# Optimization experiments

Hardware: AMD Instinct MI355X
Metric: run time of the kernel (lower is better)

## Reference

```python
import jax, jax.numpy as jnp
import numpy as np

MAX_ITER = 10
EPSILON = 1e-4


def setup_inputs() -> dict:
    key = jax.random.key(0)
    k1, k2 = jax.random.split(key)
    B, N1, N2 = 128, 512, 512
    s = jax.random.uniform(k1, (B, N1, N2), dtype=jnp.float32)
    # per-sample effective sizes; original module assumes nrows[b] == ncols[b]
    nrows = jax.random.randint(k2, (B,), 256, N1 + 1, dtype=jnp.int32)
    ncols = nrows
    return {"s": s, "nrows": nrows, "ncols": ncols}


def reference(s, nrows, ncols):
    """Faithful BiStochastic (masked Sinkhorn) forward.

    Even iter i: column-normalize within the [ncols, ncols] top-left block,
    zero everything outside the block (matches s * tmp with tmp zero outside).
    Odd  iter i: row-normalize within the [nrows, nrows] block, zero outside.
    """
    B, n1, n2 = s.shape
    i1 = jnp.arange(n1)
    i2 = jnp.arange(n2)
    # masks derived from the block-ones matrices in the original code
    cmask_r = i1[None, :] < ncols[:, None]           # [B, n1] rows < ncols
    cmask_c = i2[None, :] < ncols[:, None]           # [B, n2] cols < ncols
    rmask_r = i1[None, :] < nrows[:, None]           # [B, n1] rows < nrows
    rmask_c = i2[None, :] < nrows[:, None]           # [B, n2] cols < nrows
    col_block = cmask_r[:, :, None] & cmask_c[:, None, :]  # [B, n1, n2]
    row_block = rmask_r[:, :, None] & rmask_c[:, None, :]  # [B, n1, n2]

    s = s + EPSILON
    for i in range(MAX_ITER):
        if i % 2 == 0:
            # col_sum[b, c] = sum_{r < ncols[b]} s[b, r, c]
            col_sum = jnp.sum(jnp.where(cmask_r[:, :, None], s, 0.0),
                              axis=1, keepdims=True)          # [B, 1, n2]
            denom = jnp.where(col_block, col_sum, 1.0)
            s = jnp.where(col_block, s, 0.0) / denom
        else:
            # row_sum[b, r] = sum_{c < nrows[b]} s[b, r, c]
            row_sum = jnp.sum(jnp.where(rmask_c[:, None, :], s, 0.0),
                              axis=2, keepdims=True)          # [B, n1, 1]
            denom = jnp.where(row_block, row_sum, 1.0)
            s = jnp.where(row_block, s, 0.0) / denom
    return s
```

## Files before the change

### kernel.cpp

```cpp
#include <hip/hip_runtime.h>

#define N     512
#define NSP   4
#define SC    128
#define MROW  65
#define EPS   1e-4f

#define LDS_U   (512 * MROW + 512 + 128 * 33 + 128 + 64)
#define LDS_BYTES (LDS_U * 4)

union U32H { unsigned int u; _Float16 h[2]; };
__device__ inline float h_lo(unsigned int x){ U32H t; t.u = x; return (float)t.h[0]; }
__device__ inline float h_hi(unsigned int x){ U32H t; t.u = x; return (float)t.h[1]; }
__device__ inline unsigned int h_pk(float a, float b){ U32H t; t.h[0]=(_Float16)a; t.h[1]=(_Float16)b; return t.u; }

typedef _Float16 half2v __attribute__((ext_vector_type(2)));
#if __has_builtin(__builtin_amdgcn_fdot2)
__device__ inline float dot2(unsigned int m, unsigned int v, float c){
    return __builtin_amdgcn_fdot2(__builtin_bit_cast(half2v, m), __builtin_bit_cast(half2v, v), c, false);
}
#else
__device__ inline float dot2(unsigned int m, unsigned int v, float c){
    return c + h_lo(m)*h_lo(v) + h_hi(m)*h_hi(v);
}
#endif

__device__ inline void pass_tail(unsigned int* M2, float* red, float* vf, unsigned int* vpk,
                                 const float acc[8], int t, int part, int j, int c0, int n,
                                 int b, int sp, float* __restrict__ rp_out,
                                 float* __restrict__ vf_out) {
#pragma unroll
    for (int k = 0; k < 8; ++k) red[(8*j + k)*33 + part] = acc[k];
    __syncthreads();
    if (t < 128) {
        float s = 0.f;
#pragma unroll
        for (int p = 0; p < 32; ++p) s += red[t*33 + p];
        float v = (c0 + t < n) ? 1.f / s : 0.f;
        vf[t] = v;
        if (vf_out) vf_out[b*N + c0 + t] = v;
    }
    __syncthreads();
    if (t < 64) vpk[t] = h_pk(vf[2*t], vf[2*t+1]);
    __syncthreads();
    float p = 0.f;
    const unsigned int* row = M2 + t * MROW;
#pragma unroll
    for (int q = 0; q < 64; ++q) p = dot2(row[q], vpk[q], p);
    rp_out[((size_t)b*NSP + sp)*N + t] = p;
}

__global__ __launch_bounds__(512)
void k_pass0(const float* __restrict__ A, const int* __restrict__ nrows,
             unsigned int* __restrict__ Abf, float* __restrict__ rp_out) {
    extern __shared__ unsigned int lds[];
    unsigned int* M2 = lds;
    float* uu = (float*)(lds + 512*MROW);
    float* red = uu + 512;
    float* vf  = red + 128*33;
    unsigned int* vpk = (unsigned int*)(vf + 128);

    const int b = blockIdx.y, sp = blockIdx.x, c0 = sp * SC;
    const int n = nrows[b];
    const int t = threadIdx.x;
    const int w = t >> 6, l = t & 63;
    const int j = l & 15, rg = l >> 4;
    const size_t baseA = (size_t)b * N * N;
    const size_t baseH = (size_t)b * N * (N/2);
    const int cb = c0 + 8*j;

    bool cok[8];
#pragma unroll
    for (int k = 0; k < 8; ++k) cok[k] = (cb + k) < n;

    float acc[8] = {0,0,0,0,0,0,0,0};
    for (int it = 0; it < 16; ++it) {
        int r = it*32 + w*4 + rg;
        const float4* p = (const float4*)(A + baseA + (size_t)r*N + cb);
        float4 a0 = p[0], a1 = p[1];
        bool rok = r < n;
        float e[8];
        e[0] = (rok && cok[0]) ? a0.x + EPS : 0.f;
        e[1] = (rok && cok[1]) ? a0.y + EPS : 0.f;
        e[2] = (rok && cok[2]) ? a0.z + EPS : 0.f;
        e[3] = (rok && cok[3]) ? a0.w + EPS : 0.f;
        e[4] = (rok && cok[4]) ? a1.x + EPS : 0.f;
        e[5] = (rok && cok[5]) ? a1.y + EPS : 0.f;
        e[6] = (rok && cok[6]) ? a1.z + EPS : 0.f;
        e[7] = (rok && cok[7]) ? a1.w + EPS : 0.f;
#pragma unroll
        for (int k = 0; k < 8; ++k) acc[k] += e[k];
        uint4 q;
        q.x = h_pk(e[0], e[1]); q.y = h_pk(e[2], e[3]);
        q.z = h_pk(e[4], e[5]); q.w = h_pk(e[6], e[7]);
        *(uint4*)(Abf + baseH + (size_t)r*(N/2) + c0/2 + 4*j) = q;
        unsigned int* dst = M2 + r*MROW + 4*j;
        dst[0] = q.x; dst[1] = q.y; dst[2] = q.z; dst[3] = q.w;
    }
    (void)uu;
    pass_tail(M2, red, vf, vpk, acc, t, w*4 + rg, j, c0, n, b, sp, rp_out, nullptr);
}

__global__ __launch_bounds__(512)
void k_passN(const unsigned int* __restrict__ Abf, const int* __restrict__ nrows,
             const float* __restrict__ rp_in, float* __restrict__ rp_out,
             float* __restrict__ vf_out) {
    extern __shared__ unsigned int lds[];
    unsigned int* M2 = lds;
    float* uu = (float*)(lds + 512*MROW);
    float* red = uu + 512;
    float* vf  = red + 128*33;
    unsigned int* vpk = (unsigned int*)(vf + 128);

    const int b = blockIdx.y, sp = blockIdx.x, c0 = sp * SC;
    const int n = nrows[b];
    const int t = threadIdx.x;
    const int w = t >> 6, l = t & 63;
    const int j = l & 15, rg = l >> 4;
    const size_t baseH = (size_t)b * N * (N/2);

    {
        float s = rp_in[((size_t)b*NSP + 0)*N + t]
                + rp_in[((size_t)b*NSP + 1)*N + t]
                + rp_in[((size_t)b*NSP + 2)*N + t]
                + rp_in[((size_t)b*NSP + 3)*N + t];
        uu[t] = (t < n) ? 1.f / s : 0.f;
    }
    __syncthreads();

    float acc[8] = {0,0,0,0,0,0,0,0};
    for (int it = 0; it < 16; ++it) {
        int r = it*32 + w*4 + rg;
        uint4 q = *(const uint4*)(Abf + baseH + (size_t)r*(N/2) + c0/2 + 4*j);
        float ur = uu[r];
        acc[0] += ur * h_lo(q.x); acc[1] += ur * h_hi(q.x);
        acc[2] += ur * h_lo(q.y); acc[3] += ur * h_hi(q.y);
        acc[4] += ur * h_lo(q.z); acc[5] += ur * h_hi(q.z);
        acc[6] += ur * h_lo(q.w); acc[7] += ur * h_hi(q.w);
        unsigned int* dst = M2 + r*MROW + 4*j;
        dst[0] = q.x; dst[1] = q.y; dst[2] = q.z; dst[3] = q.w;
    }
    __syncthreads();
    pass_tail(M2, red, vf, vpk, acc, t, w*4 + rg, j, c0, n, b, sp, rp_out, vf_out);
}

__global__ __launch_bounds__(512)
void k_epi(const float* __restrict__ A, const int* __restrict__ nrows,
           const float* __restrict__ rp9, const float* __restrict__ vf8,
           float* __restrict__ out) {
    const int b = blockIdx.y;
    const int n = nrows[b];
    const int t = threadIdx.x;
    const int r = blockIdx.x*4 + (t >> 7);
    const int c = (t & 127) * 4;
    float s = rp9[((size_t)b*NSP + 0)*N + r]
            + rp9[((size_t)b*NSP + 1)*N + r]
            + rp9[((size_t)b*NSP + 2)*N + r]
            + rp9[((size_t)b*NSP + 3)*N + r];
    float ur = (r < n) ? 1.f / s : 0.f;
    float4 v = *(const float4*)(vf8 + b*N + c);
    const size_t off = (size_t)b*N*N + (size_t)r*N + c;
    float4 a = *(const float4*)(A + off);
    float4 o;
    o.x = (a.x + EPS) * ur * v.x;
    o.y = (a.y + EPS) * ur * v.y;
    o.z = (a.z + EPS) * ur * v.z;
    o.w = (a.w + EPS) * ur * v.w;
    *(float4*)(out + off) = o;
}

extern "C" void kernel_launch(void* const* d_in, const int* in_sizes, int n_in,
                              void* d_out, int out_size, void* d_ws, size_t ws_size,
                              hipStream_t stream) {
    const float* A     = (const float*)d_in[0];
    const int*   nrows = (const int*)d_in[1];
    float*       out   = (float*)d_out;
    const int    B     = in_sizes[1];

    float* rpA = (float*)d_ws;
    float* rpB = rpA + (size_t)B * NSP * N;
    float* vf8 = rpB + (size_t)B * NSP * N;
    size_t head = ((size_t)2*B*NSP*N + (size_t)B*N) * sizeof(float);
    size_t abf_bytes = (size_t)B * N * (N/2) * sizeof(unsigned int);
    unsigned int* Abf = (ws_size >= head + abf_bytes)
                      ? (unsigned int*)((char*)d_ws + head)
                      : (unsigned int*)d_out;

    hipFuncSetAttribute(reinterpret_cast<const void*>(k_pass0),
                        hipFuncAttributeMaxDynamicSharedMemorySize, LDS_BYTES);
    hipFuncSetAttribute(reinterpret_cast<const void*>(k_passN),
                        hipFuncAttributeMaxDynamicSharedMemorySize, LDS_BYTES);

    dim3 g(NSP, B);
    k_pass0<<<g, 512, LDS_BYTES, stream>>>(A, nrows, Abf, rpA);
    k_passN<<<g, 512, LDS_BYTES, stream>>>(Abf, nrows, rpA, rpB, nullptr);
    k_passN<<<g, 512, LDS_BYTES, stream>>>(Abf, nrows, rpB, rpA, nullptr);
    k_passN<<<g, 512, LDS_BYTES, stream>>>(Abf, nrows, rpA, rpB, nullptr);
    k_passN<<<g, 512, LDS_BYTES, stream>>>(Abf, nrows, rpB, rpA, vf8);
    k_epi<<<dim3(N/4, B), 512, 0, stream>>>(A, nrows, rpA, vf8, out);
}
```

Before: 319.4 us.

## Fuse Sinkhorn passes into one cooperative kernel with register-resident fp16 tile

Replaces the six-kernel sequence with one cooperative kernel that keeps each block's 512x128 fp16 slice in registers across all passes, separating passes with grid-wide syncs. It removes the repeated global reads of the fp16 copy, the LDS staging of the matrix, and the final re-read of the input in the epilogue, computing the output directly from the held values. Row partial sums now come from shuffle reductions instead of an LDS matrix-vector product. The grid of 512 blocks must all be co-resident (4 per CU with heavy register use), otherwise the launch fails and falls back to the old path. The output is now built from fp16-rounded inputs rather than the original fp32 values, which costs some precision.

Result: slower. 742.4 us (+132.4%).

```diff
diff --git a/kernel.cpp b/kernel.cpp
--- a/kernel.cpp
+++ b/kernel.cpp
@@ -1,11 +1,14 @@
 #include <hip/hip_runtime.h>
+#include <hip/hip_cooperative_groups.h>
+
+namespace cg = cooperative_groups;
 
 #define N     512
 #define NSP   4
 #define SC    128
+#define EPS   1e-4f
+
 #define MROW  65
-#define EPS   1e-4f
-
 #define LDS_U   (512 * MROW + 512 + 128 * 33 + 128 + 64)
 #define LDS_BYTES (LDS_U * 4)
 
@@ -24,6 +27,161 @@
     return c + h_lo(m)*h_lo(v) + h_hi(m)*h_hi(v);
 }
 #endif
+
+
+__device__ inline void col_reduce(float* red, float* vf, unsigned int* vpk,
+                                  const float acc[8], int t, int part, int j,
+                                  int c0, int n) {
+#pragma unroll
+    for (int k = 0; k < 8; ++k) red[(8*j + k)*33 + part] = acc[k];
+    __syncthreads();
+    if (t < 128) {
+        float s = 0.f;
+#pragma unroll
+        for (int p = 0; p < 32; ++p) s += red[t*33 + p];
+        vf[t] = (c0 + t < n) ? 1.f / s : 0.f;
+    }
+    __syncthreads();
+    if (t < 64) vpk[t] = h_pk(vf[2*t], vf[2*t+1]);
+    __syncthreads();
+}
+
+__device__ inline void row_part(const unsigned int m[16][4], const unsigned int* vpk,
+                                int j, int part, float* __restrict__ rp_dst) {
+    const unsigned int vp0 = vpk[4*j+0], vp1 = vpk[4*j+1];
+    const unsigned int vp2 = vpk[4*j+2], vp3 = vpk[4*j+3];
+    float rp[16];
+#pragma unroll
+    for (int it = 0; it < 16; ++it) {
+        float p = dot2(m[it][0], vp0, 0.f);
+        p = dot2(m[it][1], vp1, p);
+        p = dot2(m[it][2], vp2, p);
+        p = dot2(m[it][3], vp3, p);
+        rp[it] = p;
+    }
+#pragma unroll
+    for (int d = 8; d >= 1; d >>= 1) {
+        const bool up = (j & d) != 0;
+#pragma unroll
+        for (int i = 0; i < d; ++i) {
+            float send = up ? rp[i] : rp[i + d];
+            float got  = __shfl_xor(send, d, 16);
+            rp[i] = (up ? rp[i + d] : rp[i]) + got;
+        }
+    }
+    rp_dst[j*32 + part] = rp[0];
+}
+
+__global__ __launch_bounds__(512, 4)
+void k_fused(const float* __restrict__ A, const int* __restrict__ nrows,
+             float* __restrict__ rpA, float* __restrict__ rpB,
+             float* __restrict__ out) {
+    __shared__ float red[128*33];
+    __shared__ float uu[512];
+    __shared__ float vf[128];
+    __shared__ unsigned int vpk[64];
+
+    const int b = blockIdx.y, sp = blockIdx.x, c0 = sp * SC;
+    const int n = nrows[b];
+    const int t = threadIdx.x;
+    const int l = t & 63;
+    const int j = l & 15;
+    const int part = (t >> 6) * 4 + (l >> 4);
+    const size_t baseA = (size_t)b * N * N;
+    const int cb = c0 + 8*j;
+    const size_t rpOff = ((size_t)b * NSP + sp) * N;
+    const size_t rpB0  = (size_t)b * NSP * N;
+    cg::grid_group grid = cg::this_grid();
+
+    bool cok[8];
+#pragma unroll
+    for (int k = 0; k < 8; ++k) cok[k] = (cb + k) < n;
+
+    unsigned int m[16][4];
+    {
+        float acc[8] = {0,0,0,0,0,0,0,0};
+#pragma unroll
+        for (int it = 0; it < 16; ++it) {
+            const int r = it*32 + part;
+            const float4* p = (const float4*)(A + baseA + (size_t)r*N + cb);
+            float4 a0 = p[0], a1 = p[1];
+            const bool rok = r < n;
+            float e[8];
+            e[0] = (rok & cok[0]) ? a0.x + EPS : 0.f;
+            e[1] = (rok & cok[1]) ? a0.y + EPS : 0.f;
+            e[2] = (rok & cok[2]) ? a0.z + EPS : 0.f;
+            e[3] = (rok & cok[3]) ? a0.w + EPS : 0.f;
+            e[4] = (rok & cok[4]) ? a1.x + EPS : 0.f;
+            e[5] = (rok & cok[5]) ? a1.y + EPS : 0.f;
+            e[6] = (rok & cok[6]) ? a1.z + EPS : 0.f;
+            e[7] = (rok & cok[7]) ? a1.w + EPS : 0.f;
+#pragma unroll
+            for (int k = 0; k < 8; ++k) acc[k] += e[k];
+            m[it][0] = h_pk(e[0], e[1]);
+            m[it][1] = h_pk(e[2], e[3]);
+            m[it][2] = h_pk(e[4], e[5]);
+            m[it][3] = h_pk(e[6], e[7]);
+        }
+        col_reduce(red, vf, vpk, acc, t, part, j, c0, n);
+    }
+    row_part(m, vpk, j, part, rpA + rpOff);
+    grid.sync();
+
+    auto do_pass = [&](const float* __restrict__ rIn, float* __restrict__ rOut) {
+        {
+            float s = rIn[rpB0 + 0*N + t] + rIn[rpB0 + 1*N + t]
+                    + rIn[rpB0 + 2*N + t] + rIn[rpB0 + 3*N + t];
+            uu[t] = (t < n) ? 1.f / s : 0.f;
+        }
+        __syncthreads();
+        float acc[8] = {0,0,0,0,0,0,0,0};
+#pragma unroll
+        for (int it = 0; it < 16; ++it) {
+            const float ur = uu[it*32 + part];
+            acc[0] += ur * h_lo(m[it][0]);
+            acc[1] += ur * h_hi(m[it][0]);
+            acc[2] += ur * h_lo(m[it][1]);
+            acc[3] += ur * h_hi(m[it][1]);
+            acc[4] += ur * h_lo(m[it][2]);
+            acc[5] += ur * h_hi(m[it][2]);
+            acc[6] += ur * h_lo(m[it][3]);
+            acc[7] += ur * h_hi(m[it][3]);
+        }
+        col_reduce(red, vf, vpk, acc, t, part, j, c0, n);
+        row_part(m, vpk, j, part, rOut + rpOff);
+        grid.sync();
+    };
+    do_pass(rpA, rpB);
+    do_pass(rpB, rpA);
+    do_pass(rpA, rpB);
+    do_pass(rpB, rpA);
+
+    {
+        float s = rpA[rpB0 + 0*N + t] + rpA[rpB0 + 1*N + t]
+                + rpA[rpB0 + 2*N + t] + rpA[rpB0 + 3*N + t];
+        uu[t] = (t < n) ? 1.f / s : 0.f;
+    }
+    __syncthreads();
+    const float v0 = vf[8*j+0], v1 = vf[8*j+1], v2 = vf[8*j+2], v3 = vf[8*j+3];
+    const float v4 = vf[8*j+4], v5 = vf[8*j+5], v6 = vf[8*j+6], v7 = vf[8*j+7];
+#pragma unroll
+    for (int it = 0; it < 16; ++it) {
+        const int r = it*32 + part;
+        const float ur = uu[r];
+        float4 o0, o1;
+        o0.x = h_lo(m[it][0]) * ur * v0;
+        o0.y = h_hi(m[it][0]) * ur * v1;
+        o0.z = h_lo(m[it][1]) * ur * v2;
+        o0.w = h_hi(m[it][1]) * ur * v3;
+        o1.x = h_lo(m[it][2]) * ur * v4;
+        o1.y = h_hi(m[it][2]) * ur * v5;
+        o1.z = h_lo(m[it][3]) * ur * v6;
+        o1.w = h_hi(m[it][3]) * ur * v7;
+        float4* q = (float4*)(out + baseA + (size_t)r*N + cb);
+        q[0] = o0; q[1] = o1;
+    }
+}
+
 
 __device__ inline void pass_tail(unsigned int* M2, float* red, float* vf, unsigned int* vpk,
                                  const float acc[8], int t, int part, int j, int c0, int n,
@@ -180,6 +338,15 @@
     float* rpA = (float*)d_ws;
     float* rpB = rpA + (size_t)B * NSP * N;
     float* vf8 = rpB + (size_t)B * NSP * N;
+
+    {
+        void* args[] = { (void*)&A, (void*)&nrows, (void*)&rpA, (void*)&rpB, (void*)&out };
+        hipError_t err = hipLaunchCooperativeKernel(
+            reinterpret_cast<const void*>(&k_fused),
+            dim3(NSP, B), dim3(512), args, 0, stream);
+        if (err == hipSuccess) return;
+    }
+
     size_t head = ((size_t)2*B*NSP*N + (size_t)B*N) * sizeof(float);
     size_t abf_bytes = (size_t)B * N * (N/2) * sizeof(unsigned int);
     unsigned int* Abf = (ws_size >= head + abf_bytes)
```
